# Kernel tuning notes

Hardware: AMD Instinct MI355X
Metric: run time of the kernel (lower is better)

## Reference

```python
import jax, jax.numpy as jnp
import numpy as np

NEG_SLOPE = 0.2
BN_EPS = 1e-5


def _gat(x, src, dst, W, a_src, a_dst, b, concat):
    """PyG GATConv (eval mode, self-loops already in src/dst)."""
    N = x.shape[0]
    H, C = a_src.shape
    h = (x @ W).reshape(N, H, C)                      # [N,H,C]
    s = (h * a_src).sum(-1)                           # [N,H] per-node src score
    d = (h * a_dst).sum(-1)                           # [N,H] per-node dst score
    e = jax.nn.leaky_relu(s[src] + d[dst], NEG_SLOPE)  # [E,H]
    m = jax.ops.segment_max(e, dst, num_segments=N)   # segment softmax over dst
    ex = jnp.exp(e - m[dst])
    denom = jax.ops.segment_sum(ex, dst, num_segments=N)
    alpha = ex / denom[dst]                           # [E,H]
    out = jax.ops.segment_sum(alpha[:, :, None] * h[src], dst, num_segments=N)  # [N,H,C]
    out = out.reshape(N, H * C) if concat else out.mean(axis=1)
    return out + b


def _bn(x, g, beta, rm, rv):
    return (x - rm) * (g / jnp.sqrt(rv + BN_EPS)) + beta


def setup_inputs() -> dict:
    key = jax.random.key(0)
    ks = jax.random.split(key, 32)
    N, E, IN, HID, H, NC = 50000, 400000, 768, 128, 4, 2
    d = {}
    d['x'] = jax.random.normal(ks[0], (N, IN), jnp.float32)
    d['edge_index'] = jax.random.randint(ks[1], (2, E), 0, N, jnp.int64)

    def lin(k, fan_in, shape):
        return jax.random.normal(k, shape, jnp.float32) * (1.0 / np.sqrt(fan_in))

    # layer 1: in=768 -> 4 heads x 128, concat
    d['W1'] = lin(ks[2], IN, (IN, H * HID)); d['a1s'] = lin(ks[3], HID, (H, HID))
    d['a1d'] = lin(ks[4], HID, (H, HID)); d['b1'] = jnp.zeros((H * HID,), jnp.float32)
    d['g1'] = jax.random.uniform(ks[5], (H * HID,), jnp.float32, 0.5, 1.5)
    d['be1'] = jax.random.normal(ks[6], (H * HID,), jnp.float32) * 0.1
    d['rm1'] = jax.random.normal(ks[7], (H * HID,), jnp.float32) * 0.1
    d['rv1'] = jax.random.uniform(ks[8], (H * HID,), jnp.float32, 0.5, 1.5)
    d['W2'] = lin(ks[9], H * HID, (H * HID, H * HID)); d['a2s'] = lin(ks[10], HID, (H, HID))
    d['a2d'] = lin(ks[11], HID, (H, HID)); d['b2'] = jnp.zeros((H * HID,), jnp.float32)
    d['g2'] = jax.random.uniform(ks[12], (H * HID,), jnp.float32, 0.5, 1.5)
    d['be2'] = jax.random.normal(ks[13], (H * HID,), jnp.float32) * 0.1
    d['rm2'] = jax.random.normal(ks[14], (H * HID,), jnp.float32) * 0.1
    d['rv2'] = jax.random.uniform(ks[15], (H * HID,), jnp.float32, 0.5, 1.5)
    # layer 3: 512 -> 1 head x 128, mean (concat=False)
    d['W3'] = lin(ks[16], H * HID, (H * HID, HID)); d['a3s'] = lin(ks[17], HID, (1, HID))
    d['a3d'] = lin(ks[18], HID, (1, HID)); d['b3'] = jnp.zeros((HID,), jnp.float32)
    d['g3'] = jax.random.uniform(ks[19], (HID,), jnp.float32, 0.5, 1.5)
    d['be3'] = jax.random.normal(ks[20], (HID,), jnp.float32) * 0.1
    d['rm3'] = jax.random.normal(ks[21], (HID,), jnp.float32) * 0.1
    d['rv3'] = jax.random.uniform(ks[22], (HID,), jnp.float32, 0.5, 1.5)
    # classifier 128 -> 2
    d['Wc'] = lin(ks[23], HID, (HID, NC)); d['bc'] = jnp.zeros((NC,), jnp.float32)
    return d


def reference(x, edge_index, W1, a1s, a1d, b1, g1, be1, rm1, rv1,
              W2, a2s, a2d, b2, g2, be2, rm2, rv2,
              W3, a3s, a3d, b3, g3, be3, rm3, rv3, Wc, bc):
    N = x.shape[0]
    loops = jnp.arange(N, dtype=edge_index.dtype)  # GATConv add_self_loops=True
    src = jnp.concatenate([edge_index[0], loops])
    dst = jnp.concatenate([edge_index[1], loops])

    h = _gat(x, src, dst, W1, a1s, a1d, b1, concat=True)
    h = jax.nn.elu(_bn(h, g1, be1, rm1, rv1))          # dropout: eval mode (identity)
    h = _gat(h, src, dst, W2, a2s, a2d, b2, concat=True)
    h = jax.nn.elu(_bn(h, g2, be2, rm2, rv2))
    h = _gat(h, src, dst, W3, a3s, a3d, b3, concat=False)
    h = jax.nn.elu(_bn(h, g3, be3, rm3, rv3))
    return h @ Wc + bc                                  # [N, 2] logits
```

## Files before the change

kernel.cpp:

```cpp
#include <hip/hip_runtime.h>
#include <hip/hip_bf16.h>
#include <math.h>

constexpr int IN_F = 768;
constexpr float NEG_SLOPE = 0.2f;
constexpr float BN_EPS = 1e-5f;

typedef __attribute__((ext_vector_type(8))) short short8;
typedef __attribute__((ext_vector_type(4))) float f32x4;

__device__ inline float bf2f(unsigned short u) {
    unsigned int x = ((unsigned int)u) << 16;
    return __uint_as_float(x);
}
__device__ inline unsigned short f2bf(float f) {
    __hip_bfloat16 h = __float2bfloat16(f);
    return *(unsigned short*)&h;
}
__device__ inline void gload_lds16(const unsigned short* g, unsigned short* l) {
    __builtin_amdgcn_global_load_lds(
        (const __attribute__((address_space(1))) void*)g,
        (__attribute__((address_space(3))) void*)l, 16, 0, 0);
}


__global__ void init_counts(int* __restrict__ count, int* __restrict__ cursor, int N) {
    int i = blockIdx.x * blockDim.x + threadIdx.x;
    if (i < N) { count[i] = 1; cursor[i] = 0; }
}

__global__ void count_edges(const int* __restrict__ dst, int E, int* __restrict__ count) {
    int e = blockIdx.x * blockDim.x + threadIdx.x;
    if (e < E) atomicAdd(&count[dst[e]], 1);
}

__global__ void scan_counts(const int* __restrict__ count, int* __restrict__ row_start, int N) {
    __shared__ int wsum[17];
    __shared__ int carry;
    int tid = threadIdx.x;
    int lane = tid & 63, w = tid >> 6;
    if (tid == 0) carry = 0;
    __syncthreads();
    for (int base = 0; base < N; base += 4096) {
        int idx = base + tid * 4;
        int v0 = (idx + 0 < N) ? count[idx + 0] : 0;
        int v1 = (idx + 1 < N) ? count[idx + 1] : 0;
        int v2 = (idx + 2 < N) ? count[idx + 2] : 0;
        int v3 = (idx + 3 < N) ? count[idx + 3] : 0;
        int tsum = v0 + v1 + v2 + v3;
        int x = tsum;
        #pragma unroll
        for (int off = 1; off < 64; off <<= 1) {
            int y = __shfl_up(x, off, 64);
            if (lane >= off) x += y;
        }
        if (lane == 63) wsum[w] = x;
        __syncthreads();
        if (tid == 0) {
            int r = 0;
            for (int i = 0; i < 16; i++) { int t = wsum[i]; wsum[i] = r; r += t; }
            wsum[16] = r;
        }
        __syncthreads();
        int excl = carry + wsum[w] + (x - tsum);
        if (idx + 0 < N) row_start[idx + 0] = excl;
        if (idx + 1 < N) row_start[idx + 1] = excl + v0;
        if (idx + 2 < N) row_start[idx + 2] = excl + v0 + v1;
        if (idx + 3 < N) row_start[idx + 3] = excl + v0 + v1 + v2;
        __syncthreads();
        if (tid == 0) carry += wsum[16];
        __syncthreads();
    }
    if (tid == 0) row_start[N] = carry;
}

__global__ void scatter_edges(const int* __restrict__ srcA, const int* __restrict__ dstA,
                              int E, int N, const int* __restrict__ row_start,
                              int* __restrict__ cursor, int* __restrict__ col,
                              int* __restrict__ dstn) {
    int i = blockIdx.x * blockDim.x + threadIdx.x;
    if (i < E) {
        int d = dstA[i];
        int pos = row_start[d] + atomicAdd(&cursor[d], 1);
        col[pos] = srcA[i];
        dstn[pos] = d;
    } else if (i < E + N) {
        int n = i - E;
        int pos = row_start[n] + atomicAdd(&cursor[n], 1);
        col[pos] = n;
        dstn[pos] = n;
    }
}


__global__ void cast_x_bf16(const float* __restrict__ x, unsigned short* __restrict__ xb,
                            long total) {
    long i = ((long)blockIdx.x * blockDim.x + threadIdx.x) * 4;
    if (i >= total) return;
    float4 v = *(const float4*)&x[i];
    *(ushort2*)&xb[i] = make_ushort2(f2bf(v.x), f2bf(v.y));
    *(ushort2*)&xb[i + 2] = make_ushort2(f2bf(v.z), f2bf(v.w));
}

__global__ void cast_transpose_w(const float* __restrict__ W, unsigned short* __restrict__ Wt,
                                 int K, int Ncols) {
    int idx = blockIdx.x * blockDim.x + threadIdx.x;
    if (idx >= K * Ncols) return;
    int k = idx / Ncols, n = idx % Ncols;
    Wt[(size_t)n * K + k] = f2bf(W[idx]);
}


__global__ __launch_bounds__(256) void gemm_bf16(const unsigned short* __restrict__ A,
                                                 const unsigned short* __restrict__ Wt,
                                                 unsigned short* __restrict__ C,
                                                 int M, int Nc, int K) {
    __shared__ __align__(16) unsigned short As[128 * 32];
    __shared__ __align__(16) unsigned short Bs[128 * 32];
    const int tid = threadIdx.x;
    const int lane = tid & 63;
    const int wave = tid >> 6;
    const int wm = wave >> 1, wn = wave & 1;
    const int row0 = blockIdx.x * 128, col0 = blockIdx.y * 128;

    f32x4 acc[4][4];
    #pragma unroll
    for (int i = 0; i < 4; i++)
        #pragma unroll
        for (int j = 0; j < 4; j++)
            acc[i][j] = (f32x4){0.f, 0.f, 0.f, 0.f};

    const int ldm = tid >> 2;
    const int kpart = (tid & 3) * 8;
    const int khalf = (lane >> 4) * 8;
    const int fr = lane & 15;

    for (int k0 = 0; k0 < K; k0 += 32) {
        __syncthreads();
        #pragma unroll
        for (int i = 0; i < 2; i++) {
            int gr = row0 + i * 64 + ldm; if (gr >= M) gr = M - 1;
            gload_lds16(A + (size_t)gr * K + k0 + kpart, &As[i * 2048 + tid * 8]);
            int n = col0 + i * 64 + ldm;
            gload_lds16(Wt + (size_t)n * K + k0 + kpart, &Bs[i * 2048 + tid * 8]);
        }
        __syncthreads();
        short8 a[4], b[4];
        #pragma unroll
        for (int t = 0; t < 4; t++) {
            a[t] = *(const short8*)&As[(wm * 64 + t * 16 + fr) * 32 + khalf];
            b[t] = *(const short8*)&Bs[(wn * 64 + t * 16 + fr) * 32 + khalf];
        }
        #pragma unroll
        for (int mi = 0; mi < 4; mi++)
            #pragma unroll
            for (int ni = 0; ni < 4; ni++)
                acc[mi][ni] = __builtin_amdgcn_mfma_f32_16x16x32_bf16(
                    a[mi], b[ni], acc[mi][ni], 0, 0, 0);
    }

    const int rbase = row0 + wm * 64 + (lane >> 4) * 4;
    const int cbase = col0 + wn * 64 + fr;
    #pragma unroll
    for (int mi = 0; mi < 4; mi++) {
        #pragma unroll
        for (int reg = 0; reg < 4; reg++) {
            int r = rbase + mi * 16 + reg;
            if (r < M) {
                #pragma unroll
                for (int ni = 0; ni < 4; ni++)
                    C[(size_t)r * Nc + cbase + ni * 16] = f2bf(acc[mi][ni][reg]);
            }
        }
    }
}


template <int H>
__global__ void node_scores_v(const unsigned short* __restrict__ h,
                              const float* __restrict__ a_s, const float* __restrict__ a_d,
                              float* __restrict__ s, float* __restrict__ d, int N) {
    int lane = threadIdx.x & 63;
    int wv = threadIdx.x >> 6;
    int n = blockIdx.x * 4 + wv;
    if (n >= N) return;
    if (H == 4) {
        int ch0 = lane * 8;
        uint4 raw = *(const uint4*)&h[(size_t)n * 512 + ch0];
        float4 as0 = *(const float4*)&a_s[ch0];
        float4 as1 = *(const float4*)&a_s[ch0 + 4];
        float4 ad0 = *(const float4*)&a_d[ch0];
        float4 ad1 = *(const float4*)&a_d[ch0 + 4];
        float v0 = bf2f((unsigned short)(raw.x & 0xffff)), v1 = bf2f((unsigned short)(raw.x >> 16));
        float v2 = bf2f((unsigned short)(raw.y & 0xffff)), v3 = bf2f((unsigned short)(raw.y >> 16));
        float v4 = bf2f((unsigned short)(raw.z & 0xffff)), v5 = bf2f((unsigned short)(raw.z >> 16));
        float v6 = bf2f((unsigned short)(raw.w & 0xffff)), v7 = bf2f((unsigned short)(raw.w >> 16));
        float ps = v0 * as0.x + v1 * as0.y + v2 * as0.z + v3 * as0.w
                 + v4 * as1.x + v5 * as1.y + v6 * as1.z + v7 * as1.w;
        float pd = v0 * ad0.x + v1 * ad0.y + v2 * ad0.z + v3 * ad0.w
                 + v4 * ad1.x + v5 * ad1.y + v6 * ad1.z + v7 * ad1.w;
        #pragma unroll
        for (int off = 8; off >= 1; off >>= 1) {
            ps += __shfl_xor(ps, off, 64);
            pd += __shfl_xor(pd, off, 64);
        }
        if ((lane & 15) == 0) {
            int hh = lane >> 4;
            s[n * 4 + hh] = ps;
            d[n * 4 + hh] = pd;
        }
    } else {
        int c = lane * 2;
        unsigned int raw = *(const unsigned int*)&h[(size_t)n * 128 + c];
        float v0 = bf2f((unsigned short)(raw & 0xffff));
        float v1 = bf2f((unsigned short)(raw >> 16));
        float ps = v0 * a_s[c] + v1 * a_s[c + 1];
        float pd = v0 * a_d[c] + v1 * a_d[c + 1];
        #pragma unroll
        for (int off = 32; off >= 1; off >>= 1) {
            ps += __shfl_xor(ps, off, 64);
            pd += __shfl_xor(pd, off, 64);
        }
        if (lane == 0) { s[n] = ps; d[n] = pd; }
    }
}


template <int H>
__global__ void edge_weights(const int* __restrict__ col, const int* __restrict__ dstn,
                             const float* __restrict__ s, const float* __restrict__ d,
                             float* __restrict__ wgt, int P) {
    int p = blockIdx.x * blockDim.x + threadIdx.x;
    if (p >= P) return;
    int sn = col[p], dn = dstn[p];
    if (H == 4) {
        float4 sv = *(const float4*)&s[sn * 4];
        float4 dv = *(const float4*)&d[dn * 4];
        float4 o;
        float e;
        e = sv.x + dv.x; e = e > 0.f ? e : NEG_SLOPE * e; o.x = __expf(e);
        e = sv.y + dv.y; e = e > 0.f ? e : NEG_SLOPE * e; o.y = __expf(e);
        e = sv.z + dv.z; e = e > 0.f ? e : NEG_SLOPE * e; o.z = __expf(e);
        e = sv.w + dv.w; e = e > 0.f ? e : NEG_SLOPE * e; o.w = __expf(e);
        *(float4*)&wgt[p * 4] = o;
    } else {
        float e = s[sn] + d[dn];
        e = e > 0.f ? e : NEG_SLOPE * e;
        wgt[p] = __expf(e);
    }
}


__global__ void gat_agg_h4(const unsigned short* __restrict__ h, const float* __restrict__ wgt,
                           const int* __restrict__ row_start, const int* __restrict__ col,
                           const float* __restrict__ bias,
                           const float* __restrict__ gam, const float* __restrict__ beta,
                           const float* __restrict__ rm, const float* __restrict__ rv,
                           unsigned short* __restrict__ out, int N) {
    int lane = threadIdx.x & 63;
    int wv = threadIdx.x >> 6;
    int n = blockIdx.x * 4 + wv;
    if (n >= N) return;
    int beg = row_start[n], end = row_start[n + 1];
    int hh = lane >> 4;
    int ch0 = lane * 8;

    float acc[8] = {0.f, 0.f, 0.f, 0.f, 0.f, 0.f, 0.f, 0.f};
    float denom = 0.f;

    for (int i = beg; i < end; i += 8) {
        uint4 raw[8]; float w[8];
        #pragma unroll
        for (int u = 0; u < 8; u++) {
            int e0 = i + u;
            int e = e0 < end ? e0 : end - 1;
            int sn = col[e];
            w[u] = (e0 < end) ? wgt[e * 4 + hh] : 0.f;
            raw[u] = *(const uint4*)&h[(size_t)sn * 512 + ch0];
        }
        #pragma unroll
        for (int u = 0; u < 8; u++) {
            denom += w[u];
            acc[0] += w[u] * bf2f((unsigned short)(raw[u].x & 0xffff));
            acc[1] += w[u] * bf2f((unsigned short)(raw[u].x >> 16));
            acc[2] += w[u] * bf2f((unsigned short)(raw[u].y & 0xffff));
            acc[3] += w[u] * bf2f((unsigned short)(raw[u].y >> 16));
            acc[4] += w[u] * bf2f((unsigned short)(raw[u].z & 0xffff));
            acc[5] += w[u] * bf2f((unsigned short)(raw[u].z >> 16));
            acc[6] += w[u] * bf2f((unsigned short)(raw[u].w & 0xffff));
            acc[7] += w[u] * bf2f((unsigned short)(raw[u].w >> 16));
        }
    }
    float inv = 1.f / denom;
    float v[8];
    #pragma unroll
    for (int c = 0; c < 8; c++) {
        int ch = ch0 + c;
        float t = acc[c] * inv + bias[ch];
        t = (t - rm[ch]) * (gam[ch] * rsqrtf(rv[ch] + BN_EPS)) + beta[ch];
        v[c] = t > 0.f ? t : expf(t) - 1.f;
    }
    uint4 p;
    p.x = (unsigned int)f2bf(v[0]) | ((unsigned int)f2bf(v[1]) << 16);
    p.y = (unsigned int)f2bf(v[2]) | ((unsigned int)f2bf(v[3]) << 16);
    p.z = (unsigned int)f2bf(v[4]) | ((unsigned int)f2bf(v[5]) << 16);
    p.w = (unsigned int)f2bf(v[6]) | ((unsigned int)f2bf(v[7]) << 16);
    *(uint4*)&out[(size_t)n * 512 + ch0] = p;
}


__global__ void gat_agg_h1(const unsigned short* __restrict__ h, const float* __restrict__ wgt,
                           const int* __restrict__ row_start, const int* __restrict__ col,
                           const float* __restrict__ bias,
                           const float* __restrict__ gam, const float* __restrict__ beta,
                           const float* __restrict__ rm, const float* __restrict__ rv,
                           float* __restrict__ out, int N) {
    int lane = threadIdx.x & 63;
    int wv = threadIdx.x >> 6;
    int n = blockIdx.x * 4 + wv;
    if (n >= N) return;
    int beg = row_start[n], end = row_start[n + 1];
    int q = lane >> 4;
    int fl = lane & 15;
    const size_t hoff = fl * 8;

    float acc[8] = {0.f, 0.f, 0.f, 0.f, 0.f, 0.f, 0.f, 0.f};
    float denom = 0.f;

    for (int i = beg; i < end; i += 16) {
        uint4 raw[4]; float w[4];
        #pragma unroll
        for (int u = 0; u < 4; u++) {
            int e0 = i + u * 4 + q;
            int e = e0 < end ? e0 : end - 1;
            int sn = col[e];
            w[u] = (e0 < end) ? wgt[e] : 0.f;
            raw[u] = *(const uint4*)&h[(size_t)sn * 128 + hoff];
        }
        #pragma unroll
        for (int u = 0; u < 4; u++) {
            denom += w[u];
            acc[0] += w[u] * bf2f((unsigned short)(raw[u].x & 0xffff));
            acc[1] += w[u] * bf2f((unsigned short)(raw[u].x >> 16));
            acc[2] += w[u] * bf2f((unsigned short)(raw[u].y & 0xffff));
            acc[3] += w[u] * bf2f((unsigned short)(raw[u].y >> 16));
            acc[4] += w[u] * bf2f((unsigned short)(raw[u].z & 0xffff));
            acc[5] += w[u] * bf2f((unsigned short)(raw[u].z >> 16));
            acc[6] += w[u] * bf2f((unsigned short)(raw[u].w & 0xffff));
            acc[7] += w[u] * bf2f((unsigned short)(raw[u].w >> 16));
        }
    }
    #pragma unroll
    for (int c = 0; c < 8; c++) {
        acc[c] += __shfl_xor(acc[c], 16, 64);
        acc[c] += __shfl_xor(acc[c], 32, 64);
    }
    denom += __shfl_xor(denom, 16, 64);
    denom += __shfl_xor(denom, 32, 64);

    if (q == 0) {
        float inv = 1.f / denom;
        int ch0 = fl * 8;
        float v[8];
        #pragma unroll
        for (int c = 0; c < 8; c++) {
            int ch = ch0 + c;
            float t = acc[c] * inv + bias[ch];
            t = (t - rm[ch]) * (gam[ch] * rsqrtf(rv[ch] + BN_EPS)) + beta[ch];
            v[c] = t > 0.f ? t : expf(t) - 1.f;
        }
        float* o = out + (size_t)n * 128 + ch0;
        *(float4*)&o[0] = make_float4(v[0], v[1], v[2], v[3]);
        *(float4*)&o[4] = make_float4(v[4], v[5], v[6], v[7]);
    }
}


__global__ void classifier_k(const float* __restrict__ a, const float* __restrict__ Wc,
                             const float* __restrict__ bc, float* __restrict__ out, int N) {
    int lane = threadIdx.x & 63;
    int w = threadIdx.x >> 6;
    int n = blockIdx.x * 4 + w;
    if (n >= N) return;
    float v0 = a[(size_t)n * 128 + lane];
    float v1 = a[(size_t)n * 128 + 64 + lane];
    float p0 = v0 * Wc[lane * 2 + 0] + v1 * Wc[(64 + lane) * 2 + 0];
    float p1 = v0 * Wc[lane * 2 + 1] + v1 * Wc[(64 + lane) * 2 + 1];
    #pragma unroll
    for (int off = 32; off >= 1; off >>= 1) {
        p0 += __shfl_xor(p0, off, 64);
        p1 += __shfl_xor(p1, off, 64);
    }
    if (lane == 0) {
        out[n * 2 + 0] = p0 + bc[0];
        out[n * 2 + 1] = p1 + bc[1];
    }
}


extern "C" void kernel_launch(void* const* d_in, const int* in_sizes, int n_in,
                              void* d_out, int out_size, void* d_ws, size_t ws_size,
                              hipStream_t stream) {
    const float* x   = (const float*)d_in[0];
    const int*   ei  = (const int*)d_in[1];
    const float* W1  = (const float*)d_in[2];
    const float* a1s = (const float*)d_in[3];
    const float* a1d = (const float*)d_in[4];
    const float* b1  = (const float*)d_in[5];
    const float* gm1 = (const float*)d_in[6];
    const float* be1 = (const float*)d_in[7];
    const float* rm1 = (const float*)d_in[8];
    const float* rv1 = (const float*)d_in[9];
    const float* W2  = (const float*)d_in[10];
    const float* a2s = (const float*)d_in[11];
    const float* a2d = (const float*)d_in[12];
    const float* b2  = (const float*)d_in[13];
    const float* gm2 = (const float*)d_in[14];
    const float* be2 = (const float*)d_in[15];
    const float* rm2 = (const float*)d_in[16];
    const float* rv2 = (const float*)d_in[17];
    const float* W3  = (const float*)d_in[18];
    const float* a3s = (const float*)d_in[19];
    const float* a3d = (const float*)d_in[20];
    const float* b3  = (const float*)d_in[21];
    const float* gm3 = (const float*)d_in[22];
    const float* be3 = (const float*)d_in[23];
    const float* rm3 = (const float*)d_in[24];
    const float* rv3 = (const float*)d_in[25];
    const float* Wc  = (const float*)d_in[26];
    const float* bc  = (const float*)d_in[27];

    int N = in_sizes[0] / IN_F;
    int E = in_sizes[1] / 2;
    int P = E + N;
    const int* srcA = ei;
    const int* dstA = ei + E;

    unsigned short* xb   = (unsigned short*)d_ws;
    unsigned short* hbuf = xb + (size_t)N * 768;
    unsigned short* gbuf = hbuf + (size_t)N * 512;
    float* sbuf = (float*)(gbuf + (size_t)N * 512);
    float* dbuf = sbuf + (size_t)N * 4;
    float* wgt  = dbuf + (size_t)N * 4;
    unsigned short* Wt1 = (unsigned short*)(wgt + (size_t)P * 4);
    unsigned short* Wt2 = Wt1 + 512 * 768;
    unsigned short* Wt3 = Wt2 + 512 * 512;
    int* count     = (int*)(Wt3 + 128 * 512);
    int* cursor    = count + N;
    int* row_start = cursor + N;
    int* col       = row_start + N + 1;
    int* dstn      = col + P;
    float* o3 = (float*)xb;

    init_counts<<<(N + 255) / 256, 256, 0, stream>>>(count, cursor, N);
    count_edges<<<(E + 255) / 256, 256, 0, stream>>>(dstA, E, count);
    scan_counts<<<1, 1024, 0, stream>>>(count, row_start, N);
    scatter_edges<<<(E + N + 255) / 256, 256, 0, stream>>>(srcA, dstA, E, N, row_start,
                                                           cursor, col, dstn);
    long xtot = (long)N * IN_F;
    cast_x_bf16<<<(int)((xtot / 4 + 255) / 256), 256, 0, stream>>>(x, xb, xtot);
    cast_transpose_w<<<(768 * 512 + 255) / 256, 256, 0, stream>>>(W1, Wt1, 768, 512);
    cast_transpose_w<<<(512 * 512 + 255) / 256, 256, 0, stream>>>(W2, Wt2, 512, 512);
    cast_transpose_w<<<(512 * 128 + 255) / 256, 256, 0, stream>>>(W3, Wt3, 512, 128);

    int Mb = (N + 127) / 128;
    int Nb4 = (N + 3) / 4;

    gemm_bf16<<<dim3(Mb, 4), 256, 0, stream>>>(xb, Wt1, hbuf, N, 512, 768);
    node_scores_v<4><<<Nb4, 256, 0, stream>>>(hbuf, a1s, a1d, sbuf, dbuf, N);
    edge_weights<4><<<(P + 255) / 256, 256, 0, stream>>>(col, dstn, sbuf, dbuf, wgt, P);
    gat_agg_h4<<<Nb4, 256, 0, stream>>>(hbuf, wgt, row_start, col,
                                        b1, gm1, be1, rm1, rv1, gbuf, N);
    gemm_bf16<<<dim3(Mb, 4), 256, 0, stream>>>(gbuf, Wt2, hbuf, N, 512, 512);
    node_scores_v<4><<<Nb4, 256, 0, stream>>>(hbuf, a2s, a2d, sbuf, dbuf, N);
    edge_weights<4><<<(P + 255) / 256, 256, 0, stream>>>(col, dstn, sbuf, dbuf, wgt, P);
    gat_agg_h4<<<Nb4, 256, 0, stream>>>(hbuf, wgt, row_start, col,
                                        b2, gm2, be2, rm2, rv2, gbuf, N);
    gemm_bf16<<<dim3(Mb, 1), 256, 0, stream>>>(gbuf, Wt3, hbuf, N, 128, 512);
    node_scores_v<1><<<Nb4, 256, 0, stream>>>(hbuf, a3s, a3d, sbuf, dbuf, N);
    edge_weights<1><<<(P + 255) / 256, 256, 0, stream>>>(col, dstn, sbuf, dbuf, wgt, P);
    gat_agg_h1<<<Nb4, 256, 0, stream>>>(hbuf, wgt, row_start, col,
                                        b3, gm3, be3, rm3, rv3, o3, N);
    classifier_k<<<Nb4, 256, 0, stream>>>(o3, Wc, bc, (float*)d_out, N);
}
```

Before: 743.3 us.

## Fuse attention score dot-products into GEMM epilogue and classifier into final aggregation

The per-node source/destination attention scores are now computed in the GEMM epilogue from fp32 accumulators. Each wave reduces its 64-column half-head slice with shuffles and writes partial sums, which edge_weights adds together. This removes three node_scores launches and the re-read of the bf16 feature matrix. The classifier is folded into the last aggregation kernel, and the GEMM grid is transposed so column blocks of one row tile run adjacently. The cost is a heavier epilogue in the GEMM and twice the score storage read per edge. Scores now come from fp32 values instead of bf16-rounded ones.

After: 733.3 us. About the same (-1.4%).

```diff
diff --git a/kernel.cpp b/kernel.cpp
--- a/kernel.cpp
+++ b/kernel.cpp
@@ -114,14 +114,18 @@
 __global__ __launch_bounds__(256) void gemm_bf16(const unsigned short* __restrict__ A,
                                                  const unsigned short* __restrict__ Wt,
                                                  unsigned short* __restrict__ C,
-                                                 int M, int Nc, int K) {
+                                                 const float* __restrict__ a_s,
+                                                 const float* __restrict__ a_d,
+                                                 float* __restrict__ s2, float* __restrict__ d2,
+                                                 int M, int Nc, int K, int H) {
     __shared__ __align__(16) unsigned short As[128 * 32];
     __shared__ __align__(16) unsigned short Bs[128 * 32];
     const int tid = threadIdx.x;
     const int lane = tid & 63;
     const int wave = tid >> 6;
     const int wm = wave >> 1, wn = wave & 1;
-    const int row0 = blockIdx.x * 128, col0 = blockIdx.y * 128;
+    const int by = blockIdx.x;
+    const int row0 = blockIdx.y * 128, col0 = by * 128;
 
     f32x4 acc[4][4];
     #pragma unroll
@@ -134,6 +138,7 @@
     const int kpart = (tid & 3) * 8;
     const int khalf = (lane >> 4) * 8;
     const int fr = lane & 15;
+    const int quad = lane >> 4;
 
     for (int k0 = 0; k0 < K; k0 += 32) {
         __syncthreads();
@@ -159,7 +164,7 @@
                     a[mi], b[ni], acc[mi][ni], 0, 0, 0);
     }
 
-    const int rbase = row0 + wm * 64 + (lane >> 4) * 4;
+    const int rbase = row0 + wm * 64 + quad * 4;
     const int cbase = col0 + wn * 64 + fr;
     #pragma unroll
     for (int mi = 0; mi < 4; mi++) {
@@ -173,78 +178,72 @@
             }
         }
     }
-}
-
-
-template <int H>
-__global__ void node_scores_v(const unsigned short* __restrict__ h,
-                              const float* __restrict__ a_s, const float* __restrict__ a_d,
-                              float* __restrict__ s, float* __restrict__ d, int N) {
-    int lane = threadIdx.x & 63;
-    int wv = threadIdx.x >> 6;
-    int n = blockIdx.x * 4 + wv;
-    if (n >= N) return;
-    if (H == 4) {
-        int ch0 = lane * 8;
-        uint4 raw = *(const uint4*)&h[(size_t)n * 512 + ch0];
-        float4 as0 = *(const float4*)&a_s[ch0];
-        float4 as1 = *(const float4*)&a_s[ch0 + 4];
-        float4 ad0 = *(const float4*)&a_d[ch0];
-        float4 ad1 = *(const float4*)&a_d[ch0 + 4];
-        float v0 = bf2f((unsigned short)(raw.x & 0xffff)), v1 = bf2f((unsigned short)(raw.x >> 16));
-        float v2 = bf2f((unsigned short)(raw.y & 0xffff)), v3 = bf2f((unsigned short)(raw.y >> 16));
-        float v4 = bf2f((unsigned short)(raw.z & 0xffff)), v5 = bf2f((unsigned short)(raw.z >> 16));
-        float v6 = bf2f((unsigned short)(raw.w & 0xffff)), v7 = bf2f((unsigned short)(raw.w >> 16));
-        float ps = v0 * as0.x + v1 * as0.y + v2 * as0.z + v3 * as0.w
-                 + v4 * as1.x + v5 * as1.y + v6 * as1.z + v7 * as1.w;
-        float pd = v0 * ad0.x + v1 * ad0.y + v2 * ad0.z + v3 * ad0.w
-                 + v4 * ad1.x + v5 * ad1.y + v6 * ad1.z + v7 * ad1.w;
-        #pragma unroll
-        for (int off = 8; off >= 1; off >>= 1) {
-            ps += __shfl_xor(ps, off, 64);
-            pd += __shfl_xor(pd, off, 64);
-        }
-        if ((lane & 15) == 0) {
-            int hh = lane >> 4;
-            s[n * 4 + hh] = ps;
-            d[n * 4 + hh] = pd;
-        }
-    } else {
-        int c = lane * 2;
-        unsigned int raw = *(const unsigned int*)&h[(size_t)n * 128 + c];
-        float v0 = bf2f((unsigned short)(raw & 0xffff));
-        float v1 = bf2f((unsigned short)(raw >> 16));
-        float ps = v0 * a_s[c] + v1 * a_s[c + 1];
-        float pd = v0 * a_d[c] + v1 * a_d[c + 1];
-        #pragma unroll
-        for (int off = 32; off >= 1; off >>= 1) {
-            ps += __shfl_xor(ps, off, 64);
-            pd += __shfl_xor(pd, off, 64);
-        }
-        if (lane == 0) { s[n] = ps; d[n] = pd; }
+
+    float asv[4], adv[4];
+    #pragma unroll
+    for (int ni = 0; ni < 4; ni++) {
+        int c = by * 128 + wn * 64 + ni * 16 + fr;
+        asv[ni] = a_s[c];
+        adv[ni] = a_d[c];
+    }
+    float ps[4][4], pd[4][4];
+    #pragma unroll
+    for (int mi = 0; mi < 4; mi++)
+        #pragma unroll
+        for (int reg = 0; reg < 4; reg++) {
+            float t = 0.f, u = 0.f;
+            #pragma unroll
+            for (int ni = 0; ni < 4; ni++) {
+                t += acc[mi][ni][reg] * asv[ni];
+                u += acc[mi][ni][reg] * adv[ni];
+            }
+            ps[mi][reg] = t;
+            pd[mi][reg] = u;
+        }
+    #pragma unroll
+    for (int off = 1; off <= 8; off <<= 1)
+        #pragma unroll
+        for (int mi = 0; mi < 4; mi++)
+            #pragma unroll
+            for (int reg = 0; reg < 4; reg++) {
+                ps[mi][reg] += __shfl_xor(ps[mi][reg], off, 64);
+                pd[mi][reg] += __shfl_xor(pd[mi][reg], off, 64);
+            }
+    float oS = 0.f, oD = 0.f;
+    #pragma unroll
+    for (int mi = 0; mi < 4; mi++)
+        #pragma unroll
+        for (int reg = 0; reg < 4; reg++)
+            if (fr == mi * 4 + reg) { oS = ps[mi][reg]; oD = pd[mi][reg]; }
+    int rw = rbase + (fr >> 2) * 16 + (fr & 3);
+    if (rw < M) {
+        s2[(size_t)rw * (2 * H) + wn * H + by] = oS;
+        d2[(size_t)rw * (2 * H) + wn * H + by] = oD;
     }
 }
 
 
 template <int H>
 __global__ void edge_weights(const int* __restrict__ col, const int* __restrict__ dstn,
-                             const float* __restrict__ s, const float* __restrict__ d,
+                             const float* __restrict__ s2, const float* __restrict__ d2,
                              float* __restrict__ wgt, int P) {
     int p = blockIdx.x * blockDim.x + threadIdx.x;
     if (p >= P) return;
     int sn = col[p], dn = dstn[p];
     if (H == 4) {
-        float4 sv = *(const float4*)&s[sn * 4];
-        float4 dv = *(const float4*)&d[dn * 4];
+        float4 sa = *(const float4*)&s2[sn * 8];
+        float4 sb = *(const float4*)&s2[sn * 8 + 4];
+        float4 da = *(const float4*)&d2[dn * 8];
+        float4 db = *(const float4*)&d2[dn * 8 + 4];
         float4 o;
         float e;
-        e = sv.x + dv.x; e = e > 0.f ? e : NEG_SLOPE * e; o.x = __expf(e);
-        e = sv.y + dv.y; e = e > 0.f ? e : NEG_SLOPE * e; o.y = __expf(e);
-        e = sv.z + dv.z; e = e > 0.f ? e : NEG_SLOPE * e; o.z = __expf(e);
-        e = sv.w + dv.w; e = e > 0.f ? e : NEG_SLOPE * e; o.w = __expf(e);
+        e = sa.x + sb.x + da.x + db.x; e = e > 0.f ? e : NEG_SLOPE * e; o.x = __expf(e);
+        e = sa.y + sb.y + da.y + db.y; e = e > 0.f ? e : NEG_SLOPE * e; o.y = __expf(e);
+        e = sa.z + sb.z + da.z + db.z; e = e > 0.f ? e : NEG_SLOPE * e; o.z = __expf(e);
+        e = sa.w + sb.w + da.w + db.w; e = e > 0.f ? e : NEG_SLOPE * e; o.w = __expf(e);
         *(float4*)&wgt[p * 4] = o;
     } else {
-        float e = s[sn] + d[dn];
+        float e = s2[sn * 2] + s2[sn * 2 + 1] + d2[dn * 2] + d2[dn * 2 + 1];
         e = e > 0.f ? e : NEG_SLOPE * e;
         wgt[p] = __expf(e);
     }
@@ -309,12 +308,13 @@
 }
 
 
-__global__ void gat_agg_h1(const unsigned short* __restrict__ h, const float* __restrict__ wgt,
-                           const int* __restrict__ row_start, const int* __restrict__ col,
-                           const float* __restrict__ bias,
-                           const float* __restrict__ gam, const float* __restrict__ beta,
-                           const float* __restrict__ rm, const float* __restrict__ rv,
-                           float* __restrict__ out, int N) {
+__global__ void gat_agg_h1_cls(const unsigned short* __restrict__ h, const float* __restrict__ wgt,
+                               const int* __restrict__ row_start, const int* __restrict__ col,
+                               const float* __restrict__ bias,
+                               const float* __restrict__ gam, const float* __restrict__ beta,
+                               const float* __restrict__ rm, const float* __restrict__ rv,
+                               const float* __restrict__ Wc, const float* __restrict__ bc,
+                               float* __restrict__ out, int N) {
     int lane = threadIdx.x & 63;
     int wv = threadIdx.x >> 6;
     int n = blockIdx.x * 4 + wv;
@@ -361,39 +361,25 @@
     if (q == 0) {
         float inv = 1.f / denom;
         int ch0 = fl * 8;
-        float v[8];
+        float p0 = 0.f, p1 = 0.f;
         #pragma unroll
         for (int c = 0; c < 8; c++) {
             int ch = ch0 + c;
             float t = acc[c] * inv + bias[ch];
             t = (t - rm[ch]) * (gam[ch] * rsqrtf(rv[ch] + BN_EPS)) + beta[ch];
-            v[c] = t > 0.f ? t : expf(t) - 1.f;
-        }
-        float* o = out + (size_t)n * 128 + ch0;
-        *(float4*)&o[0] = make_float4(v[0], v[1], v[2], v[3]);
-        *(float4*)&o[4] = make_float4(v[4], v[5], v[6], v[7]);
-    }
-}
-
-
-__global__ void classifier_k(const float* __restrict__ a, const float* __restrict__ Wc,
-                             const float* __restrict__ bc, float* __restrict__ out, int N) {
-    int lane = threadIdx.x & 63;
-    int w = threadIdx.x >> 6;
-    int n = blockIdx.x * 4 + w;
-    if (n >= N) return;
-    float v0 = a[(size_t)n * 128 + lane];
-    float v1 = a[(size_t)n * 128 + 64 + lane];
-    float p0 = v0 * Wc[lane * 2 + 0] + v1 * Wc[(64 + lane) * 2 + 0];
-    float p1 = v0 * Wc[lane * 2 + 1] + v1 * Wc[(64 + lane) * 2 + 1];
-    #pragma unroll
-    for (int off = 32; off >= 1; off >>= 1) {
-        p0 += __shfl_xor(p0, off, 64);
-        p1 += __shfl_xor(p1, off, 64);
-    }
-    if (lane == 0) {
-        out[n * 2 + 0] = p0 + bc[0];
-        out[n * 2 + 1] = p1 + bc[1];
+            t = t > 0.f ? t : expf(t) - 1.f;
+            p0 += t * Wc[ch * 2 + 0];
+            p1 += t * Wc[ch * 2 + 1];
+        }
+        #pragma unroll
+        for (int off = 8; off >= 1; off >>= 1) {
+            p0 += __shfl_xor(p0, off, 64);
+            p1 += __shfl_xor(p1, off, 64);
+        }
+        if (fl == 0) {
+            out[n * 2 + 0] = p0 + bc[0];
+            out[n * 2 + 1] = p1 + bc[1];
+        }
     }
 }
 
@@ -439,9 +425,9 @@
     unsigned short* xb   = (unsigned short*)d_ws;
     unsigned short* hbuf = xb + (size_t)N * 768;
     unsigned short* gbuf = hbuf + (size_t)N * 512;
-    float* sbuf = (float*)(gbuf + (size_t)N * 512);
-    float* dbuf = sbuf + (size_t)N * 4;
-    float* wgt  = dbuf + (size_t)N * 4;
+    float* s2   = (float*)(gbuf + (size_t)N * 512);
+    float* d2   = s2 + (size_t)N * 8;
+    float* wgt  = d2 + (size_t)N * 8;
     unsigned short* Wt1 = (unsigned short*)(wgt + (size_t)P * 4);
     unsigned short* Wt2 = Wt1 + 512 * 768;
     unsigned short* Wt3 = Wt2 + 512 * 512;
@@ -450,7 +436,6 @@
     int* row_start = cursor + N;
     int* col       = row_start + N + 1;
     int* dstn      = col + P;
-    float* o3 = (float*)xb;
 
     init_counts<<<(N + 255) / 256, 256, 0, stream>>>(count, cursor, N);
     count_edges<<<(E + 255) / 256, 256, 0, stream>>>(dstA, E, count);
@@ -466,20 +451,16 @@
     int Mb = (N + 127) / 128;
     int Nb4 = (N + 3) / 4;
 
-    gemm_bf16<<<dim3(Mb, 4), 256, 0, stream>>>(xb, Wt1, hbuf, N, 512, 768);
-    node_scores_v<4><<<Nb4, 256, 0, stream>>>(hbuf, a1s, a1d, sbuf, dbuf, N);
-    edge_weights<4><<<(P + 255) / 256, 256, 0, stream>>>(col, dstn, sbuf, dbuf, wgt, P);
+    gemm_bf16<<<dim3(4, Mb), 256, 0, stream>>>(xb, Wt1, hbuf, a1s, a1d, s2, d2, N, 512, 768, 4);
+    edge_weights<4><<<(P + 255) / 256, 256, 0, stream>>>(col, dstn, s2, d2, wgt, P);
     gat_agg_h4<<<Nb4, 256, 0, stream>>>(hbuf, wgt, row_start, col,
                                         b1, gm1, be1, rm1, rv1, gbuf, N);
-    gemm_bf16<<<dim3(Mb, 4), 256, 0, stream>>>(gbuf, Wt2, hbuf, N, 512, 512);
-    node_scores_v<4><<<Nb4, 256, 0, stream>>>(hbuf, a2s, a2d, sbuf, dbuf, N);
-    edge_weights<4><<<(P + 255) / 256, 256, 0, stream>>>(col, dstn, sbuf, dbuf, wgt, P);
+    gemm_bf16<<<dim3(4, Mb), 256, 0, stream>>>(gbuf, Wt2, hbuf, a2s, a2d, s2, d2, N, 512, 512, 4);
+    edge_weights<4><<<(P + 255) / 256, 256, 0, stream>>>(col, dstn, s2, d2, wgt, P);
     gat_agg_h4<<<Nb4, 256, 0, stream>>>(hbuf, wgt, row_start, col,
                                         b2, gm2, be2, rm2, rv2, gbuf, N);
-    gemm_bf16<<<dim3(Mb, 1), 256, 0, stream>>>(gbuf, Wt3, hbuf, N, 128, 512);
-    node_scores_v<1><<<Nb4, 256, 0, stream>>>(hbuf, a3s, a3d, sbuf, dbuf, N);
-    edge_weights<1><<<(P + 255) / 256, 256, 0, stream>>>(col, dstn, sbuf, dbuf, wgt, P);
-    gat_agg_h1<<<Nb4, 256, 0, stream>>>(hbuf, wgt, row_start, col,
-                                        b3, gm3, be3, rm3, rv3, o3, N);
-    classifier_k<<<Nb4, 256, 0, stream>>>(o3, Wc, bc, (float*)d_out, N);
-}
+    gemm_bf16<<<dim3(1, Mb), 256, 0, stream>>>(gbuf, Wt3, hbuf, a3s, a3d, s2, d2, N, 128, 512, 1);
+    edge_weights<1><<<(P + 255) / 256, 256, 0, stream>>>(col, dstn, s2, d2, wgt, P);
+    gat_agg_h1_cls<<<Nb4, 256, 0, stream>>>(hbuf, wgt, row_start, col,
+                                            b3, gm3, be3, rm3, rv3, Wc, bc, (float*)d_out, N);
+}
```
